# Kernel tuning notes

Hardware: AMD Instinct MI355X
Metric: run time of the kernel (lower is better)

The kernel has to match this reference:

```python
import jax, jax.numpy as jnp
import numpy as np

NPOINT = 512
NSAMPLE = 32
RADIUS = 0.2


def furthest_point_sampling(pts, npoint):
    # pts: (B, N, 3) -> (B, npoint) int32 indices
    B, N, _ = pts.shape

    def step(carry, _):
        dist, far = carry  # (B,N), (B,)
        centroid = jnp.take_along_axis(pts, far[:, None, None], axis=1)  # (B,1,3)
        d2 = jnp.sum((pts - centroid) ** 2, axis=-1)  # (B,N)
        dist = jnp.minimum(dist, d2)
        nfar = jnp.argmax(dist, axis=-1).astype(jnp.int32)
        return (dist, nfar), far

    init = (jnp.full((B, N), 1e10, pts.dtype), jnp.zeros((B,), jnp.int32))
    _, idxs = jax.lax.scan(step, init, None, length=npoint)
    return idxs.T  # (B, npoint)


def ball_query(new_xyz, xyz, nsample, radius):
    # new_xyz: (B,S,3), xyz: (B,N,3) -> (B,S,nsample) int32
    N = xyz.shape[1]
    d2 = jnp.sum((new_xyz[:, :, None, :] - xyz[:, None, :, :]) ** 2, axis=-1)  # (B,S,N)
    ar = jnp.arange(N, dtype=jnp.int32)
    key = jnp.where(d2 < radius * radius, ar, N)  # valid idx, else sentinel N
    idx = jnp.sort(key, axis=-1)[..., :nsample]  # first nsample in-radius indices
    first = idx[..., :1]
    idx = jnp.where(idx == N, first, idx)  # pad with first valid (CUDA ball_query behavior)
    return jnp.minimum(idx, N - 1)


def group_points(feat, idx):
    # feat: (B,C,N), idx: (B,S,K) -> (B,C,S,K)
    return jax.vmap(lambda f, i: f[:, i])(feat, idx)


def pointnet_sa(xyz, features, W1, b1, W2, b2, W3, b3):
    xyz_t = jnp.transpose(xyz, (0, 2, 1))  # (B,N,3)
    fps_idx = furthest_point_sampling(xyz_t, NPOINT)  # (B,S)
    new_xyz = group_points(xyz, fps_idx[:, :, None])[..., 0]  # (B,3,S)
    idx = ball_query(jnp.transpose(new_xyz, (0, 2, 1)), xyz_t, NSAMPLE, RADIUS)  # (B,S,K)
    grouped_xyz = group_points(xyz, idx) - new_xyz[:, :, :, None]  # (B,3,S,K), centered
    grouped_feat = group_points(features, idx)  # (B,C,S,K)
    h = jnp.concatenate([grouped_xyz, grouped_feat], axis=1)  # (B,C+3,S,K)
    for W, b in ((W1, b1), (W2, b2), (W3, b3)):
        h = jax.nn.relu(jnp.einsum('oc,bcsk->bosk', W, h) + b[None, :, None, None])
    new_features = jnp.max(h, axis=3)  # (B,out,S)
    return new_xyz, new_features


def setup_inputs() -> dict:
    key = jax.random.key(0)
    ks = jax.random.split(key, 8)
    B, N, C = 16, 2048, 64
    return {
        'xyz': jax.random.uniform(ks[0], (B, 3, N), dtype=jnp.float32),
        'features': jax.random.normal(ks[1], (B, C, N), dtype=jnp.float32),
        'W1': jax.random.normal(ks[2], (64, 67), dtype=jnp.float32) * 0.1,
        'b1': jnp.zeros((64,), jnp.float32),
        'W2': jax.random.normal(ks[3], (128, 64), dtype=jnp.float32) * 0.1,
        'b2': jnp.zeros((128,), jnp.float32),
        'W3': jax.random.normal(ks[4], (256, 128), dtype=jnp.float32) * 0.1,
        'b3': jnp.zeros((256,), jnp.float32),
    }


def reference(xyz, features, W1, b1, W2, b2, W3, b3):
    return pointnet_sa(xyz, features, W1, b1, W2, b2, W3, b3)
```

## Files before the change

### kernel.cpp

```cpp
#include <hip/hip_runtime.h>

#define NB 16
#define NN 2048
#define NP 512
#define NS 32
#define NC 64
#define NWORK 496

typedef _Float16 f16x8 __attribute__((ext_vector_type(8)));
typedef _Float16 f16x4 __attribute__((ext_vector_type(4)));
typedef float f32x4 __attribute__((ext_vector_type(4)));
typedef float f32x2 __attribute__((ext_vector_type(2)));

__device__ __forceinline__ float sqdist(float dx, float dy, float dz) {
  return __fadd_rn(__fadd_rn(__fmul_rn(dx, dx), __fmul_rn(dy, dy)), __fmul_rn(dz, dz));
}

__device__ __forceinline__ f32x2 pk_add(f32x2 a, f32x2 b) {
  f32x2 d;
  asm("v_pk_add_f32 %0, %1, %2" : "=v"(d) : "v"(a), "v"(b));
  return d;
}
__device__ __forceinline__ f32x2 pk_mul(f32x2 a, f32x2 b) {
  f32x2 d;
  asm("v_pk_mul_f32 %0, %1, %2" : "=v"(d) : "v"(a), "v"(b));
  return d;
}

template <int CTRL>
__device__ __forceinline__ float dppmaxf(float m) {
  int t = __builtin_amdgcn_update_dpp(0, __float_as_int(m), CTRL, 0xf, 0xf, true);
  return fmaxf(m, __int_as_float(t));
}

__device__ __forceinline__ unsigned ld_relax(const unsigned* p) {
  return __hip_atomic_load(p, __ATOMIC_RELAXED, __HIP_MEMORY_SCOPE_AGENT);
}
__device__ __forceinline__ void waitge(const unsigned* p, unsigned need) {
  if (ld_relax(p) < need) {
    unsigned spins = 0;
    while (ld_relax(p) < need) {
      __builtin_amdgcn_s_sleep(8);
      if (++spins > (1u << 22)) break;
    }
  }
  (void)__hip_atomic_load(p, __ATOMIC_ACQUIRE, __HIP_MEMORY_SCOPE_AGENT);
}

__global__ void init_kernel(unsigned* ctr) {
  if (threadIdx.x < 18) ctr[threadIdx.x * 16] = 0;
}

#define HSTR 104
#define A1STR 72
#define A2STR 136
#define A1OFF 17408

__global__ __launch_bounds__(256, 2) void fused_kernel(
    const float* __restrict__ xyz, const float* __restrict__ feat,
    const float* __restrict__ W1, const float* __restrict__ b1, const float* __restrict__ W2,
    const float* __restrict__ b2, const float* __restrict__ W3, const float* __restrict__ b3,
    float* __restrict__ out, _Float16* __restrict__ featF, float* __restrict__ xyzT,
    _Float16* __restrict__ W1f, _Float16* __restrict__ W2f, _Float16* __restrict__ W3f,
    unsigned* __restrict__ ctr) {
  __shared__ __align__(16) char sm[53824];
  __shared__ unsigned mitem;
  const int bid = blockIdx.x;
  const int t = threadIdx.x;
  float* newxyz = out;

  if (bid < NB) {
    const int b = bid;
    const int w = t >> 6;
    const float* X = xyz + (size_t)b * 3 * NN;
    float4* XL = (float4*)sm;
    uint2* ck = (uint2*)(sm + 32768);

    f32x2 px[4], py[4], pz[4], dist[4];
#pragma unroll
    for (int jj = 0; jj < 4; ++jj) {
      int n0 = t + 256 * jj, n1 = n0 + 1024;
      px[jj] = f32x2{X[n0], X[n1]};
      py[jj] = f32x2{X[NN + n0], X[NN + n1]};
      pz[jj] = f32x2{X[2 * NN + n0], X[2 * NN + n1]};
      dist[jj] = f32x2{1e10f, 1e10f};
      XL[n0] = make_float4(px[jj].x, py[jj].x, pz[jj].x, 0.f);
      XL[n1] = make_float4(px[jj].y, py[jj].y, pz[jj].y, 0.f);
    }
    float cx = X[0], cy = X[NN], cz = X[2 * NN];
    __syncthreads();
    int buf = 0;
    for (int i = 0; i < NP; ++i) {
      if (t == 0) {
        __hip_atomic_store(&newxyz[b * 3 * NP + i], cx, __ATOMIC_RELAXED,
                           __HIP_MEMORY_SCOPE_AGENT);
        __hip_atomic_store(&newxyz[b * 3 * NP + NP + i], cy, __ATOMIC_RELAXED,
                           __HIP_MEMORY_SCOPE_AGENT);
        __hip_atomic_store(&newxyz[b * 3 * NP + 2 * NP + i], cz, __ATOMIC_RELAXED,
                           __HIP_MEMORY_SCOPE_AGENT);
        if ((i & 63) == 63)
          __hip_atomic_store(&ctr[b * 16], (unsigned)(i + 1), __ATOMIC_RELEASE,
                             __HIP_MEMORY_SCOPE_AGENT);
      }
      const f32x2 ncx = f32x2{-cx, -cx}, ncy = f32x2{-cy, -cy}, ncz = f32x2{-cz, -cz};
      float hm[4];
#pragma unroll
      for (int jj = 0; jj < 4; ++jj) {
        f32x2 dx = pk_add(px[jj], ncx);
        f32x2 dy = pk_add(py[jj], ncy);
        f32x2 dz = pk_add(pz[jj], ncz);
        f32x2 s = pk_add(pk_add(pk_mul(dx, dx), pk_mul(dy, dy)), pk_mul(dz, dz));
        f32x2 d = dist[jj];
        d.x = fminf(d.x, s.x);
        d.y = fminf(d.y, s.y);
        dist[jj] = d;
        hm[jj] = fmaxf(d.x, d.y);
      }
      float m = fmaxf(fmaxf(hm[0], hm[1]), fmaxf(hm[2], hm[3]));
      m = dppmaxf<0x111>(m);
      m = dppmaxf<0x112>(m);
      m = dppmaxf<0x114>(m);
      m = dppmaxf<0x118>(m);
      m = dppmaxf<0x142>(m);
      m = dppmaxf<0x143>(m);
      const float vmax = __int_as_float(__builtin_amdgcn_readlane(__float_as_int(m), 63));
      unsigned long long mm[8];
#pragma unroll
      for (int jj = 0; jj < 4; ++jj) {
        mm[jj] = __ballot(dist[jj].x == vmax);
        mm[4 + jj] = __ballot(dist[jj].y == vmax);
      }
      unsigned nw = 0;
#pragma unroll
      for (int q = 7; q >= 0; --q)
        if (mm[q]) nw = 256u * (unsigned)q + (unsigned)(w << 6) + (unsigned)__builtin_ctzll(mm[q]);
      if ((t & 63) == 0) ck[buf * 4 + w] = make_uint2(__float_as_uint(vmax), nw);
      __syncthreads();
      uint4 c01 = *(const uint4*)&ck[buf * 4 + 0];
      uint4 c23 = *(const uint4*)&ck[buf * 4 + 2];
      unsigned v = c01.x, n = c01.y;
      if (c01.z > v || (c01.z == v && c01.w < n)) { v = c01.z; n = c01.w; }
      if (c23.x > v || (c23.x == v && c23.y < n)) { v = c23.x; n = c23.y; }
      if (c23.z > v || (c23.z == v && c23.w < n)) { v = c23.z; n = c23.w; }
      float4 c = XL[n];
      cx = c.x;
      cy = c.y;
      cz = c.z;
      buf ^= 1;
    }
  } else {
    const int wid = bid - NB;
    for (int rep = 0; rep < 2; ++rep) {
      int p = wid + rep * NWORK;
      if (p >= 512) break;
      float(*tile)[65] = (float(*)[65])sm;
      const int b = p >> 5;
      const int n0 = (p & 31) * 64;
      const int g = t >> 6, l = t & 63;
      if (g == 0) {
        int n = n0 + l;
        float4 q;
        q.x = xyz[(size_t)b * 3 * NN + n];
        q.y = xyz[(size_t)b * 3 * NN + NN + n];
        q.z = xyz[(size_t)b * 3 * NN + 2 * NN + n];
        q.w = 0.f;
        ((float4*)xyzT)[(size_t)b * NN + n] = q;
      }
      __syncthreads();
#pragma unroll
      for (int r = 0; r < 16; ++r) {
        int c = g * 16 + r;
        tile[c][l] = feat[((size_t)b * NC + c) * NN + n0 + l];
      }
      __syncthreads();
#pragma unroll
      for (int r = 0; r < 16; ++r) {
        int nl = g * 16 + r;
        featF[((size_t)(b * NN + n0 + nl)) * NC + l] = (_Float16)tile[l][nl];
      }
    }
    if (wid == 31) {
      for (int i = t; i < 256 * 128; i += 256) {
        if (i < 64 * 96) {
          int o = i / 96, k = i - o * 96;
          float v = (k < 64) ? W1[o * 67 + 3 + k] : ((k < 67) ? W1[o * 67 + (k - 64)] : 0.f);
          W1f[i] = (_Float16)v;
        }
        if (i < 128 * 64) W2f[i] = (_Float16)W2[i];
        W3f[i] = (_Float16)W3[i];
      }
    }
    __syncthreads();
    if (t == 0)
      (void)__hip_atomic_fetch_add(&ctr[16 * 16], 1u, __ATOMIC_RELEASE,
                                   __HIP_MEMORY_SCOPE_AGENT);
  }

  if (t == 0) waitge(&ctr[16 * 16], NWORK);
  __syncthreads();

  _Float16* hT = (_Float16*)sm;
  _Float16* a1T = (_Float16*)(sm) + A1OFF;
  int(*idx_l)[32] = (int(*)[32])(sm + 53248);
  float(*cxyz)[4] = (float(*)[4])(sm + 53760);
  const int lane = t & 63, w = t >> 6;
  const int cl = lane & 15;
  const int kg = lane >> 4;
  float* out2 = out + NB * 3 * NP;

  for (;;) {
    if (t == 0)
      mitem = __hip_atomic_fetch_add(&ctr[17 * 16], 1u, __ATOMIC_RELAXED,
                                     __HIP_MEMORY_SCOPE_AGENT);
    __syncthreads();
    const unsigned m = mitem;
    if (m >= (unsigned)(NB * 128)) break;
    const int b = (int)(m & 15u);
    const int sg = (int)(m >> 4);
    const int s0 = sg * 4;
    if (t == 0) waitge(&ctr[b * 16], (unsigned)(s0 + 4));
    __syncthreads();

    {
      const float* X = xyz + (size_t)b * 3 * NN;
      const int sW = s0 + w;
      const float cxw = newxyz[b * 3 * NP + sW];
      const float cyw = newxyz[b * 3 * NP + NP + sW];
      const float czw = newxyz[b * 3 * NP + 2 * NP + sW];
      if (lane == 0) {
        cxyz[w][0] = cxw;
        cxyz[w][1] = cyw;
        cxyz[w][2] = czw;
      }
      const float r2 = (float)(0.2 * 0.2);
      int total = 0, first = 0;
      bool havefirst = false;
      for (int c0 = 0; c0 < NN; c0 += 64) {
        int n = c0 + lane;
        float d2 = sqdist(X[n] - cxw, X[NN + n] - cyw, X[2 * NN + n] - czw);
        bool hit = d2 < r2;
        unsigned long long mask = __ballot(hit);
        if (!havefirst && mask) {
          first = c0 + __builtin_ctzll(mask);
          havefirst = true;
        }
        if (hit) {
          int pos = total + (int)__popcll(mask & ((1ull << lane) - 1ull));
          if (pos < NS) idx_l[w][pos] = n;
        }
        total += (int)__popcll(mask);
        if (total >= NS) break;
      }
      if (total < NS && lane >= total && lane < NS) idx_l[w][lane] = first;
    }
    __syncthreads();

    {
      const int col = t & 127, hf = t >> 7;
      const int n = idx_l[col >> 5][col & 31];
      const _Float16* F = featF + (size_t)(b * NN + n) * NC;
#pragma unroll
      for (int j = 0; j < 4; ++j) {
        int p = hf * 4 + j;
        *(f16x8*)(&hT[col * HSTR + p * 8]) = *(const f16x8*)(F + p * 8);
      }
      if (hf == 0) {
        float4 pnt = ((const float4*)xyzT)[(size_t)b * NN + n];
        f16x8 v = {};
        v[0] = (_Float16)(pnt.x - cxyz[col >> 5][0]);
        v[1] = (_Float16)(pnt.y - cxyz[col >> 5][1]);
        v[2] = (_Float16)(pnt.z - cxyz[col >> 5][2]);
        *(f16x8*)(&hT[col * HSTR + 64]) = v;
      } else {
        f16x8 z = {};
        *(f16x8*)(&hT[col * HSTR + 72]) = z;
        *(f16x8*)(&hT[col * HSTR + 80]) = z;
        *(f16x8*)(&hT[col * HSTR + 88]) = z;
      }
    }
    __syncthreads();

    {
      f32x4 acc[8];
      {
        f32x4 bb = *(const f32x4*)(b1 + w * 16 + kg * 4);
#pragma unroll
        for (int ct = 0; ct < 8; ++ct) acc[ct] = bb;
      }
#pragma unroll
      for (int ks = 0; ks < 3; ++ks) {
        f16x8 A = *(const f16x8*)(W1f + (w * 16 + cl) * 96 + ks * 32 + kg * 8);
#pragma unroll
        for (int ct = 0; ct < 8; ++ct) {
          f16x8 B = *(const f16x8*)(&hT[(ct * 16 + cl) * HSTR + ks * 32 + kg * 8]);
          acc[ct] = __builtin_amdgcn_mfma_f32_16x16x32_f16(A, B, acc[ct], 0, 0, 0);
        }
      }
#pragma unroll
      for (int ct = 0; ct < 8; ++ct) {
        f16x4 v;
#pragma unroll
        for (int i2 = 0; i2 < 4; ++i2) v[i2] = (_Float16)fmaxf(acc[ct][i2], 0.f);
        *(f16x4*)(&a1T[(ct * 16 + cl) * A1STR + w * 16 + kg * 4]) = v;
      }
    }
    __syncthreads();

    {
      f32x4 acc[2][8];
#pragma unroll
      for (int r = 0; r < 2; ++r) {
        f32x4 bb = *(const f32x4*)(b2 + w * 32 + r * 16 + kg * 4);
#pragma unroll
        for (int ct = 0; ct < 8; ++ct) acc[r][ct] = bb;
      }
#pragma unroll
      for (int ks = 0; ks < 2; ++ks) {
        f16x8 A0 = *(const f16x8*)(W2f + (w * 32 + cl) * 64 + ks * 32 + kg * 8);
        f16x8 A1 = *(const f16x8*)(W2f + (w * 32 + 16 + cl) * 64 + ks * 32 + kg * 8);
#pragma unroll
        for (int ct = 0; ct < 8; ++ct) {
          f16x8 B = *(const f16x8*)(&a1T[(ct * 16 + cl) * A1STR + ks * 32 + kg * 8]);
          acc[0][ct] = __builtin_amdgcn_mfma_f32_16x16x32_f16(A0, B, acc[0][ct], 0, 0, 0);
          acc[1][ct] = __builtin_amdgcn_mfma_f32_16x16x32_f16(A1, B, acc[1][ct], 0, 0, 0);
        }
      }
#pragma unroll
      for (int r = 0; r < 2; ++r)
#pragma unroll
        for (int ct = 0; ct < 8; ++ct) {
          f16x4 v;
#pragma unroll
          for (int i2 = 0; i2 < 4; ++i2) v[i2] = (_Float16)fmaxf(acc[r][ct][i2], 0.f);
          *(f16x4*)(&hT[(ct * 16 + cl) * A2STR + w * 32 + r * 16 + kg * 4]) = v;
        }
    }
    __syncthreads();

#pragma unroll
    for (int rh = 0; rh < 2; ++rh) {
      f32x4 acc[2][8];
#pragma unroll
      for (int r = 0; r < 2; ++r) {
        f32x4 bb = *(const f32x4*)(b3 + w * 64 + rh * 32 + r * 16 + kg * 4);
#pragma unroll
        for (int ct = 0; ct < 8; ++ct) acc[r][ct] = bb;
      }
#pragma unroll
      for (int ks = 0; ks < 4; ++ks) {
        f16x8 A0 = *(const f16x8*)(W3f + (w * 64 + rh * 32 + cl) * 128 + ks * 32 + kg * 8);
        f16x8 A1 = *(const f16x8*)(W3f + (w * 64 + rh * 32 + 16 + cl) * 128 + ks * 32 + kg * 8);
#pragma unroll
        for (int ct = 0; ct < 8; ++ct) {
          f16x8 B = *(const f16x8*)(&hT[(ct * 16 + cl) * A2STR + ks * 32 + kg * 8]);
          acc[0][ct] = __builtin_amdgcn_mfma_f32_16x16x32_f16(A0, B, acc[0][ct], 0, 0, 0);
          acc[1][ct] = __builtin_amdgcn_mfma_f32_16x16x32_f16(A1, B, acc[1][ct], 0, 0, 0);
        }
      }
#pragma unroll
      for (int r = 0; r < 2; ++r)
#pragma unroll
        for (int sl = 0; sl < 4; ++sl) {
          float vv[4];
#pragma unroll
          for (int i2 = 0; i2 < 4; ++i2) {
            float m0 = fmaxf(acc[r][sl * 2][i2], 0.f);
            float m1 = fmaxf(acc[r][sl * 2 + 1][i2], 0.f);
            float mv = fmaxf(m0, m1);
            mv = fmaxf(mv, __shfl_xor(mv, 1, 64));
            mv = fmaxf(mv, __shfl_xor(mv, 2, 64));
            mv = fmaxf(mv, __shfl_xor(mv, 4, 64));
            mv = fmaxf(mv, __shfl_xor(mv, 8, 64));
            vv[i2] = mv;
          }
          if (cl == 0) {
            int ob = w * 64 + rh * 32 + r * 16 + kg * 4;
#pragma unroll
            for (int i2 = 0; i2 < 4; ++i2)
              out2[((size_t)(b * 256 + ob + i2)) * NP + s0 + sl] = vv[i2];
          }
        }
    }
    __syncthreads();
  }
}

extern "C" void kernel_launch(void* const* d_in, const int* in_sizes, int n_in, void* d_out,
                              int out_size, void* d_ws, size_t ws_size, hipStream_t stream) {
  const float* xyz = (const float*)d_in[0];
  const float* feat = (const float*)d_in[1];
  const float* W1 = (const float*)d_in[2];
  const float* b1 = (const float*)d_in[3];
  const float* W2 = (const float*)d_in[4];
  const float* b2 = (const float*)d_in[5];
  const float* W3 = (const float*)d_in[6];
  const float* b3 = (const float*)d_in[7];
  float* out = (float*)d_out;
  char* ws = (char*)d_ws;
  float* xyzT = (float*)ws;
  _Float16* featF = (_Float16*)(ws + 524288);
  _Float16* W1f = (_Float16*)(ws + 4718592);
  _Float16* W2f = (_Float16*)(ws + 4730880);
  _Float16* W3f = (_Float16*)(ws + 4747264);
  unsigned* ctr = (unsigned*)(ws + 4812800);

  hipLaunchKernelGGL(init_kernel, dim3(1), dim3(64), 0, stream, ctr);
  hipLaunchKernelGGL(fused_kernel, dim3(512), dim3(256), 0, stream, xyz, feat, W1, b1, W2, b2, W3,
                     b3, out, featF, xyzT, W1f, W2f, W3f, ctr);
}
```

Before: 333.8 us.

## Carry winner coordinates through FPS reduction and batch centroid publishing

In the FPS loop, the winning lane now writes its own coordinates alongside its max and index, so the next centroid comes straight from the cross-wave reduction instead of a lookup in a shared-memory copy of the points. That removes the per-batch LDS point table and its setup barrier. Centroids are buffered in shared memory and flushed to global memory, with a release counter update, every 32 iterations instead of three atomic stores per iteration. The grid is also halved, with each worker block handling up to three transpose tiles, which lowers block count but adds serial work per block and an extra barrier every 32 steps.

```diff
diff --git a/kernel.cpp b/kernel.cpp
--- a/kernel.cpp
+++ b/kernel.cpp
@@ -5,7 +5,7 @@
 #define NP 512
 #define NS 32
 #define NC 64
-#define NWORK 496
+#define NWORK 240
 
 typedef _Float16 f16x8 __attribute__((ext_vector_type(8)));
 typedef _Float16 f16x4 __attribute__((ext_vector_type(4)));
@@ -73,8 +73,8 @@
     const int b = bid;
     const int w = t >> 6;
     const float* X = xyz + (size_t)b * 3 * NN;
-    float4* XL = (float4*)sm;
-    uint2* ck = (uint2*)(sm + 32768);
+    float* cst = (float*)sm;
+    unsigned* ck = (unsigned*)(sm + 6144);
 
     f32x2 px[4], py[4], pz[4], dist[4];
 #pragma unroll
@@ -84,23 +84,14 @@
       py[jj] = f32x2{X[NN + n0], X[NN + n1]};
       pz[jj] = f32x2{X[2 * NN + n0], X[2 * NN + n1]};
       dist[jj] = f32x2{1e10f, 1e10f};
-      XL[n0] = make_float4(px[jj].x, py[jj].x, pz[jj].x, 0.f);
-      XL[n1] = make_float4(px[jj].y, py[jj].y, pz[jj].y, 0.f);
     }
     float cx = X[0], cy = X[NN], cz = X[2 * NN];
-    __syncthreads();
     int buf = 0;
     for (int i = 0; i < NP; ++i) {
       if (t == 0) {
-        __hip_atomic_store(&newxyz[b * 3 * NP + i], cx, __ATOMIC_RELAXED,
-                           __HIP_MEMORY_SCOPE_AGENT);
-        __hip_atomic_store(&newxyz[b * 3 * NP + NP + i], cy, __ATOMIC_RELAXED,
-                           __HIP_MEMORY_SCOPE_AGENT);
-        __hip_atomic_store(&newxyz[b * 3 * NP + 2 * NP + i], cz, __ATOMIC_RELAXED,
-                           __HIP_MEMORY_SCOPE_AGENT);
-        if ((i & 63) == 63)
-          __hip_atomic_store(&ctr[b * 16], (unsigned)(i + 1), __ATOMIC_RELEASE,
-                             __HIP_MEMORY_SCOPE_AGENT);
+        cst[i] = cx;
+        cst[NP + i] = cy;
+        cst[2 * NP + i] = cz;
       }
       const f32x2 ncx = f32x2{-cx, -cx}, ncy = f32x2{-cy, -cy}, ncz = f32x2{-cz, -cz};
       float hm[4];
@@ -134,23 +125,70 @@
 #pragma unroll
       for (int q = 7; q >= 0; --q)
         if (mm[q]) nw = 256u * (unsigned)q + (unsigned)(w << 6) + (unsigned)__builtin_ctzll(mm[q]);
-      if ((t & 63) == 0) ck[buf * 4 + w] = make_uint2(__float_as_uint(vmax), nw);
+      const unsigned q = nw >> 8;
+      float sx = (q == 0)   ? px[0].x
+                 : (q == 1) ? px[1].x
+                 : (q == 2) ? px[2].x
+                 : (q == 3) ? px[3].x
+                 : (q == 4) ? px[0].y
+                 : (q == 5) ? px[1].y
+                 : (q == 6) ? px[2].y
+                            : px[3].y;
+      float sy = (q == 0)   ? py[0].x
+                 : (q == 1) ? py[1].x
+                 : (q == 2) ? py[2].x
+                 : (q == 3) ? py[3].x
+                 : (q == 4) ? py[0].y
+                 : (q == 5) ? py[1].y
+                 : (q == 6) ? py[2].y
+                            : py[3].y;
+      float sz = (q == 0)   ? pz[0].x
+                 : (q == 1) ? pz[1].x
+                 : (q == 2) ? pz[2].x
+                 : (q == 3) ? pz[3].x
+                 : (q == 4) ? pz[0].y
+                 : (q == 5) ? pz[1].y
+                 : (q == 6) ? pz[2].y
+                            : pz[3].y;
+      if (t == (int)(nw & 255u)) {
+        unsigned* c = ck + buf * 32 + w * 8;
+        *(uint4*)c = make_uint4(__float_as_uint(vmax), nw, __float_as_uint(sx),
+                                __float_as_uint(sy));
+        c[4] = __float_as_uint(sz);
+      }
       __syncthreads();
-      uint4 c01 = *(const uint4*)&ck[buf * 4 + 0];
-      uint4 c23 = *(const uint4*)&ck[buf * 4 + 2];
-      unsigned v = c01.x, n = c01.y;
-      if (c01.z > v || (c01.z == v && c01.w < n)) { v = c01.z; n = c01.w; }
-      if (c23.x > v || (c23.x == v && c23.y < n)) { v = c23.x; n = c23.y; }
-      if (c23.z > v || (c23.z == v && c23.w < n)) { v = c23.z; n = c23.w; }
-      float4 c = XL[n];
-      cx = c.x;
-      cy = c.y;
-      cz = c.z;
+      const unsigned* cb = ck + buf * 32;
+      uint4 a0 = *(const uint4*)(cb + 0);
+      unsigned z0 = cb[4];
+      uint4 a1 = *(const uint4*)(cb + 8);
+      unsigned z1 = cb[12];
+      uint4 a2 = *(const uint4*)(cb + 16);
+      unsigned z2 = cb[20];
+      uint4 a3 = *(const uint4*)(cb + 24);
+      unsigned z3 = cb[28];
+      unsigned k = a0.x, n = a0.y, xr = a0.z, yr = a0.w, zr = z0;
+      if (a1.x > k || (a1.x == k && a1.y < n)) { k = a1.x; n = a1.y; xr = a1.z; yr = a1.w; zr = z1; }
+      if (a2.x > k || (a2.x == k && a2.y < n)) { k = a2.x; n = a2.y; xr = a2.z; yr = a2.w; zr = z2; }
+      if (a3.x > k || (a3.x == k && a3.y < n)) { k = a3.x; n = a3.y; xr = a3.z; yr = a3.w; zr = z3; }
+      cx = __uint_as_float(xr);
+      cy = __uint_as_float(yr);
+      cz = __uint_as_float(zr);
+      if ((i & 31) == 31) {
+        if (t < 96) {
+          int coord = t >> 5, j = (i - 31) + (t & 31);
+          __hip_atomic_store(&newxyz[b * 3 * NP + coord * NP + j], cst[coord * NP + j],
+                             __ATOMIC_RELAXED, __HIP_MEMORY_SCOPE_AGENT);
+        }
+        __syncthreads();
+        if (t == 0)
+          __hip_atomic_store(&ctr[b * 16], (unsigned)(i + 1), __ATOMIC_RELEASE,
+                             __HIP_MEMORY_SCOPE_AGENT);
+      }
       buf ^= 1;
     }
   } else {
     const int wid = bid - NB;
-    for (int rep = 0; rep < 2; ++rep) {
+    for (int rep = 0; rep < 3; ++rep) {
       int p = wid + rep * NWORK;
       if (p >= 512) break;
       float(*tile)[65] = (float(*)[65])sm;
@@ -159,12 +197,12 @@
       const int g = t >> 6, l = t & 63;
       if (g == 0) {
         int n = n0 + l;
-        float4 q;
-        q.x = xyz[(size_t)b * 3 * NN + n];
-        q.y = xyz[(size_t)b * 3 * NN + NN + n];
-        q.z = xyz[(size_t)b * 3 * NN + 2 * NN + n];
-        q.w = 0.f;
-        ((float4*)xyzT)[(size_t)b * NN + n] = q;
+        float4 qd;
+        qd.x = xyz[(size_t)b * 3 * NN + n];
+        qd.y = xyz[(size_t)b * 3 * NN + NN + n];
+        qd.z = xyz[(size_t)b * 3 * NN + 2 * NN + n];
+        qd.w = 0.f;
+        ((float4*)xyzT)[(size_t)b * NN + n] = qd;
       }
       __syncthreads();
 #pragma unroll
@@ -405,6 +443,6 @@
   unsigned* ctr = (unsigned*)(ws + 4812800);
 
   hipLaunchKernelGGL(init_kernel, dim3(1), dim3(64), 0, stream, ctr);
-  hipLaunchKernelGGL(fused_kernel, dim3(512), dim3(256), 0, stream, xyz, feat, W1, b1, W2, b2, W3,
+  hipLaunchKernelGGL(fused_kernel, dim3(256), dim3(256), 0, stream, xyz, feat, W1, b1, W2, b2, W3,
                      b3, out, featF, xyzT, W1f, W2f, W3f, ctr);
 }
```

Measured after the change: 548.7 us. 1.64x slower.

## Spatially bin FPS points into cells and skip distant cell groups per iteration

Applied to the files above, without the earlier changes.

Furthest point sampling now bins each batch's points into a 4x4x4 grid in shared memory, computes bounding boxes for 16 groups of 128 points, and runs the sequential loop on a single wavefront. Each iteration skips groups whose box lower-bound distance cannot beat the previous max, avoiding per-point distance updates. Reductions use DPP min on packed keys to break ties by original index, and the whole loop runs in one wave with no block-wide barrier per iteration. The cost is extra registers (16 pairs per lane), a binning prologue, and fewer lanes active in the serial loop.

```diff
diff --git a/kernel.cpp b/kernel.cpp
--- a/kernel.cpp
+++ b/kernel.cpp
@@ -31,6 +31,11 @@
 __device__ __forceinline__ float dppmaxf(float m) {
   int t = __builtin_amdgcn_update_dpp(0, __float_as_int(m), CTRL, 0xf, 0xf, true);
   return fmaxf(m, __int_as_float(t));
+}
+template <int CTRL>
+__device__ __forceinline__ unsigned dppminu(unsigned m) {
+  int t = __builtin_amdgcn_update_dpp((int)m, (int)m, CTRL, 0xf, 0xf, false);
+  return m < (unsigned)t ? m : (unsigned)t;
 }
 
 __device__ __forceinline__ unsigned ld_relax(const unsigned* p) {
@@ -71,82 +76,158 @@
 
   if (bid < NB) {
     const int b = bid;
-    const int w = t >> 6;
     const float* X = xyz + (size_t)b * 3 * NN;
     float4* XL = (float4*)sm;
-    uint2* ck = (uint2*)(sm + 32768);
-
-    f32x2 px[4], py[4], pz[4], dist[4];
-#pragma unroll
-    for (int jj = 0; jj < 4; ++jj) {
-      int n0 = t + 256 * jj, n1 = n0 + 1024;
-      px[jj] = f32x2{X[n0], X[n1]};
-      py[jj] = f32x2{X[NN + n0], X[NN + n1]};
-      pz[jj] = f32x2{X[2 * NN + n0], X[2 * NN + n1]};
-      dist[jj] = f32x2{1e10f, 1e10f};
-      XL[n0] = make_float4(px[jj].x, py[jj].x, pz[jj].x, 0.f);
-      XL[n1] = make_float4(px[jj].y, py[jj].y, pz[jj].y, 0.f);
-    }
-    float cx = X[0], cy = X[NN], cz = X[2 * NN];
-    __syncthreads();
-    int buf = 0;
-    for (int i = 0; i < NP; ++i) {
-      if (t == 0) {
-        __hip_atomic_store(&newxyz[b * 3 * NP + i], cx, __ATOMIC_RELAXED,
-                           __HIP_MEMORY_SCOPE_AGENT);
-        __hip_atomic_store(&newxyz[b * 3 * NP + NP + i], cy, __ATOMIC_RELAXED,
-                           __HIP_MEMORY_SCOPE_AGENT);
-        __hip_atomic_store(&newxyz[b * 3 * NP + 2 * NP + i], cz, __ATOMIC_RELAXED,
-                           __HIP_MEMORY_SCOPE_AGENT);
-        if ((i & 63) == 63)
-          __hip_atomic_store(&ctr[b * 16], (unsigned)(i + 1), __ATOMIC_RELEASE,
+    unsigned* cnt = (unsigned*)(sm + 32768);
+    unsigned* off = (unsigned*)(sm + 33024);
+    float* bb = (float*)(sm + 33280);
+
+    if (t < 64) cnt[t] = 0;
+    __syncthreads();
+    unsigned mycell[8];
+    float mx[8], my[8], mz[8];
+#pragma unroll
+    for (int j2 = 0; j2 < 8; ++j2) {
+      int n = t + 256 * j2;
+      float x = X[n], y = X[NN + n], z = X[2 * NN + n];
+      mx[j2] = x; my[j2] = y; mz[j2] = z;
+      unsigned ix = min(3u, (unsigned)(x * 4.f));
+      unsigned iy = min(3u, (unsigned)(y * 4.f));
+      unsigned iz = min(3u, (unsigned)(z * 4.f));
+      mycell[j2] = (ix & 1) | ((iy & 1) << 1) | ((iz & 1) << 2) | ((ix >> 1) << 3) |
+                   ((iy >> 1) << 4) | ((iz >> 1) << 5);
+      atomicAdd(&cnt[mycell[j2]], 1u);
+    }
+    __syncthreads();
+    if (t == 0) {
+      unsigned r = 0;
+      for (int c2 = 0; c2 < 64; ++c2) {
+        off[c2] = r;
+        r += cnt[c2];
+      }
+    }
+    __syncthreads();
+#pragma unroll
+    for (int j2 = 0; j2 < 8; ++j2) {
+      int n = t + 256 * j2;
+      unsigned pos = atomicAdd(&off[mycell[j2]], 1u);
+      XL[pos] = make_float4(mx[j2], my[j2], mz[j2], __uint_as_float((unsigned)n));
+    }
+    __syncthreads();
+    if (t < 16) {
+      float lx = 3.4e38f, ly = 3.4e38f, lz = 3.4e38f;
+      float hx = -3.4e38f, hy = -3.4e38f, hz = -3.4e38f;
+      for (int q2 = 0; q2 < 128; ++q2) {
+        float4 v = XL[t * 128 + q2];
+        lx = fminf(lx, v.x); hx = fmaxf(hx, v.x);
+        ly = fminf(ly, v.y); hy = fmaxf(hy, v.y);
+        lz = fminf(lz, v.z); hz = fmaxf(hz, v.z);
+      }
+      bb[t * 6 + 0] = lx; bb[t * 6 + 1] = hx;
+      bb[t * 6 + 2] = ly; bb[t * 6 + 3] = hy;
+      bb[t * 6 + 4] = lz; bb[t * 6 + 5] = hz;
+    }
+    __syncthreads();
+
+    const int w = t >> 6;
+    if (w == 0) {
+      const int lane = t;
+      float blx, bhx, bly, bhy, blz, bhz;
+      {
+        int k = lane & 15;
+        blx = bb[k * 6 + 0]; bhx = bb[k * 6 + 1];
+        bly = bb[k * 6 + 2]; bhy = bb[k * 6 + 3];
+        blz = bb[k * 6 + 4]; bhz = bb[k * 6 + 5];
+      }
+      f32x2 px[16], py[16], pz[16], dist[16];
+      float pm[16];
+      unsigned no32[16];
+#pragma unroll
+      for (int j = 0; j < 16; ++j) {
+        float4 a = XL[j * 128 + lane * 2];
+        float4 bq = XL[j * 128 + lane * 2 + 1];
+        px[j] = f32x2{a.x, bq.x};
+        py[j] = f32x2{a.y, bq.y};
+        pz[j] = f32x2{a.z, bq.z};
+        no32[j] = (__float_as_uint(a.w) & 0xffffu) | (__float_as_uint(bq.w) << 16);
+        dist[j] = f32x2{1e10f, 1e10f};
+        pm[j] = 1e10f;
+      }
+      float cx = X[0], cy = X[NN], cz = X[2 * NN];
+      float vmaxp = 3.4e38f;
+      for (int i = 0; i < NP; ++i) {
+        if (lane == 0) {
+          __hip_atomic_store(&newxyz[b * 3 * NP + i], cx, __ATOMIC_RELAXED,
                              __HIP_MEMORY_SCOPE_AGENT);
-      }
-      const f32x2 ncx = f32x2{-cx, -cx}, ncy = f32x2{-cy, -cy}, ncz = f32x2{-cz, -cz};
-      float hm[4];
-#pragma unroll
-      for (int jj = 0; jj < 4; ++jj) {
-        f32x2 dx = pk_add(px[jj], ncx);
-        f32x2 dy = pk_add(py[jj], ncy);
-        f32x2 dz = pk_add(pz[jj], ncz);
-        f32x2 s = pk_add(pk_add(pk_mul(dx, dx), pk_mul(dy, dy)), pk_mul(dz, dz));
-        f32x2 d = dist[jj];
-        d.x = fminf(d.x, s.x);
-        d.y = fminf(d.y, s.y);
-        dist[jj] = d;
-        hm[jj] = fmaxf(d.x, d.y);
-      }
-      float m = fmaxf(fmaxf(hm[0], hm[1]), fmaxf(hm[2], hm[3]));
-      m = dppmaxf<0x111>(m);
-      m = dppmaxf<0x112>(m);
-      m = dppmaxf<0x114>(m);
-      m = dppmaxf<0x118>(m);
-      m = dppmaxf<0x142>(m);
-      m = dppmaxf<0x143>(m);
-      const float vmax = __int_as_float(__builtin_amdgcn_readlane(__float_as_int(m), 63));
-      unsigned long long mm[8];
-#pragma unroll
-      for (int jj = 0; jj < 4; ++jj) {
-        mm[jj] = __ballot(dist[jj].x == vmax);
-        mm[4 + jj] = __ballot(dist[jj].y == vmax);
-      }
-      unsigned nw = 0;
-#pragma unroll
-      for (int q = 7; q >= 0; --q)
-        if (mm[q]) nw = 256u * (unsigned)q + (unsigned)(w << 6) + (unsigned)__builtin_ctzll(mm[q]);
-      if ((t & 63) == 0) ck[buf * 4 + w] = make_uint2(__float_as_uint(vmax), nw);
-      __syncthreads();
-      uint4 c01 = *(const uint4*)&ck[buf * 4 + 0];
-      uint4 c23 = *(const uint4*)&ck[buf * 4 + 2];
-      unsigned v = c01.x, n = c01.y;
-      if (c01.z > v || (c01.z == v && c01.w < n)) { v = c01.z; n = c01.w; }
-      if (c23.x > v || (c23.x == v && c23.y < n)) { v = c23.x; n = c23.y; }
-      if (c23.z > v || (c23.z == v && c23.w < n)) { v = c23.z; n = c23.w; }
-      float4 c = XL[n];
-      cx = c.x;
-      cy = c.y;
-      cz = c.z;
-      buf ^= 1;
+          __hip_atomic_store(&newxyz[b * 3 * NP + NP + i], cy, __ATOMIC_RELAXED,
+                             __HIP_MEMORY_SCOPE_AGENT);
+          __hip_atomic_store(&newxyz[b * 3 * NP + 2 * NP + i], cz, __ATOMIC_RELAXED,
+                             __HIP_MEMORY_SCOPE_AGENT);
+          if ((i & 63) == 63)
+            __hip_atomic_store(&ctr[b * 16], (unsigned)(i + 1), __ATOMIC_RELEASE,
+                               __HIP_MEMORY_SCOPE_AGENT);
+        }
+        float ddx = fmaxf(fmaxf(blx - cx, cx - bhx), 0.f);
+        float ddy = fmaxf(fmaxf(bly - cy, cy - bhy), 0.f);
+        float ddz = fmaxf(fmaxf(blz - cz, cz - bhz), 0.f);
+        float bnd = ddx * ddx + ddy * ddy + ddz * ddz;
+        bool act = (lane < 16) && (bnd * 0.99999f < vmaxp);
+        unsigned am = (unsigned)__ballot(act);
+        const f32x2 ncx = f32x2{-cx, -cx}, ncy = f32x2{-cy, -cy}, ncz = f32x2{-cz, -cz};
+#pragma unroll
+        for (int j = 0; j < 16; ++j)
+          if (am & (1u << j)) {
+            f32x2 dx = pk_add(px[j], ncx);
+            f32x2 dy = pk_add(py[j], ncy);
+            f32x2 dz = pk_add(pz[j], ncz);
+            f32x2 s = pk_add(pk_add(pk_mul(dx, dx), pk_mul(dy, dy)), pk_mul(dz, dz));
+            f32x2 d = dist[j];
+            d.x = fminf(d.x, s.x);
+            d.y = fminf(d.y, s.y);
+            dist[j] = d;
+            pm[j] = fmaxf(d.x, d.y);
+          }
+        float m01 = fmaxf(pm[0], pm[1]), m23 = fmaxf(pm[2], pm[3]);
+        float m45 = fmaxf(pm[4], pm[5]), m67 = fmaxf(pm[6], pm[7]);
+        float m89 = fmaxf(pm[8], pm[9]), mab = fmaxf(pm[10], pm[11]);
+        float mcd = fmaxf(pm[12], pm[13]), mef = fmaxf(pm[14], pm[15]);
+        float m = fmaxf(fmaxf(fmaxf(m01, m23), fmaxf(m45, m67)),
+                        fmaxf(fmaxf(m89, mab), fmaxf(mcd, mef)));
+        m = dppmaxf<0x111>(m);
+        m = dppmaxf<0x112>(m);
+        m = dppmaxf<0x114>(m);
+        m = dppmaxf<0x118>(m);
+        m = dppmaxf<0x142>(m);
+        m = dppmaxf<0x143>(m);
+        const float vmax = __int_as_float(__builtin_amdgcn_readlane(__float_as_int(m), 63));
+        unsigned cand = 0xFFFFFFFFu;
+#pragma unroll
+        for (int j = 0; j < 16; ++j) {
+          if (__ballot(pm[j] == vmax)) {
+            unsigned base = (unsigned)(j * 128 + lane * 2);
+            unsigned k0 =
+                (dist[j].x == vmax) ? (((no32[j] & 0xffffu) << 11) | base) : 0xFFFFFFFFu;
+            unsigned k1 = (dist[j].y == vmax) ? (((no32[j] >> 16) << 11) | (base + 1u))
+                                              : 0xFFFFFFFFu;
+            unsigned kk = k0 < k1 ? k0 : k1;
+            cand = cand < kk ? cand : kk;
+          }
+        }
+        cand = dppminu<0x111>(cand);
+        cand = dppminu<0x112>(cand);
+        cand = dppminu<0x114>(cand);
+        cand = dppminu<0x118>(cand);
+        cand = dppminu<0x142>(cand);
+        cand = dppminu<0x143>(cand);
+        const unsigned key = (unsigned)__builtin_amdgcn_readlane((int)cand, 63);
+        float4 c4 = XL[key & 2047u];
+        cx = c4.x;
+        cy = c4.y;
+        cz = c4.z;
+        vmaxp = vmax;
+      }
+    } else {
+      waitge(&ctr[b * 16], (unsigned)NP);
     }
   } else {
     const int wid = bid - NB;
@@ -283,9 +364,9 @@
     {
       f32x4 acc[8];
       {
-        f32x4 bb = *(const f32x4*)(b1 + w * 16 + kg * 4);
-#pragma unroll
-        for (int ct = 0; ct < 8; ++ct) acc[ct] = bb;
+        f32x4 bb2 = *(const f32x4*)(b1 + w * 16 + kg * 4);
+#pragma unroll
+        for (int ct = 0; ct < 8; ++ct) acc[ct] = bb2;
       }
 #pragma unroll
       for (int ks = 0; ks < 3; ++ks) {
@@ -310,9 +391,9 @@
       f32x4 acc[2][8];
 #pragma unroll
       for (int r = 0; r < 2; ++r) {
-        f32x4 bb = *(const f32x4*)(b2 + w * 32 + r * 16 + kg * 4);
-#pragma unroll
-        for (int ct = 0; ct < 8; ++ct) acc[r][ct] = bb;
+        f32x4 bb2 = *(const f32x4*)(b2 + w * 32 + r * 16 + kg * 4);
+#pragma unroll
+        for (int ct = 0; ct < 8; ++ct) acc[r][ct] = bb2;
       }
 #pragma unroll
       for (int ks = 0; ks < 2; ++ks) {
@@ -342,9 +423,9 @@
       f32x4 acc[2][8];
 #pragma unroll
       for (int r = 0; r < 2; ++r) {
-        f32x4 bb = *(const f32x4*)(b3 + w * 64 + rh * 32 + r * 16 + kg * 4);
-#pragma unroll
-        for (int ct = 0; ct < 8; ++ct) acc[r][ct] = bb;
+        f32x4 bb2 = *(const f32x4*)(b3 + w * 64 + rh * 32 + r * 16 + kg * 4);
+#pragma unroll
+        for (int ct = 0; ct < 8; ++ct) acc[r][ct] = bb2;
       }
 #pragma unroll
       for (int ks = 0; ks < 4; ++ks) {
```

After: 690.1 us. +106.7%, slower.
